# Kernel tuning notes

Hardware: AMD Instinct MI355X
Metric: run time of the kernel (lower is better)

Reference implementation:

```python
import jax, jax.numpy as jnp
import numpy as np

P = 2            # power (even positive int)
TEMPERATURE = 1.0
SCALE = 1.0 / np.sqrt(64.0)  # sqrt(head_dim) scaling
EPS = 1e-6


def setup_inputs() -> dict:
    key = jax.random.key(0)
    kq, kk, kv = jax.random.split(key, 3)
    shape = (4, 16, 2048, 64)  # (B, H, N, head_dim)
    return {
        "q": jax.random.normal(kq, shape, dtype=jnp.float32),
        "k": jax.random.normal(kk, shape, dtype=jnp.float32),
        "v": jax.random.normal(kv, shape, dtype=jnp.float32),
    }


def reference(q, k, v):
    # logits = q @ k^T * scale / temperature : (B, H, N, N)
    logits = jnp.einsum("bhnd,bhmd->bhnm", q, k) * (SCALE / TEMPERATURE)
    attn = logits ** P
    attn = attn / (attn.sum(axis=-1, keepdims=True) + EPS)
    return jnp.einsum("bhnm,bhmd->bhnd", attn, v)
```

## Files before the change

### kernel.cpp

```cpp
#include <hip/hip_runtime.h>

#define N_CTX 2048
#define DHEAD 64
#define SCALE_F 0.125f
#define EPS_F 1e-6f
#define KT 64
#define NITER (N_CTX / KT)
#define QBLK 256

typedef __attribute__((ext_vector_type(8))) short short8;
typedef __attribute__((ext_vector_type(4))) short short4v;
typedef __attribute__((ext_vector_type(4))) float float4v;
typedef __attribute__((ext_vector_type(2))) unsigned uint2v;
typedef __attribute__((ext_vector_type(4))) unsigned uint4v;

#if defined(__HIP_DEVICE_COMPILE__) && __has_builtin(__builtin_amdgcn_cvt_pk_bf16_f32)
typedef __attribute__((ext_vector_type(2))) __bf16 bf16x2;
__device__ __forceinline__ unsigned pack2(float a, float b) {
    union { bf16x2 v; unsigned u; } x;
    x.v = __builtin_amdgcn_cvt_pk_bf16_f32(a, b);
    return x.u;
}
#else
__device__ __forceinline__ unsigned bf1(float f) {
    union { float f; unsigned u; } x; x.f = f;
    return (x.u + 0x7FFFu + ((x.u >> 16) & 1u)) >> 16;
}
__device__ __forceinline__ unsigned pack2(float a, float b) {
    return bf1(a) | (bf1(b) << 16);
}
#endif

#if defined(__HIP_DEVICE_COMPILE__)
  #if __has_builtin(__builtin_amdgcn_mfma_f32_16x16x16bf16_1k)
    #define MFMA16(a, b, c) __builtin_amdgcn_mfma_f32_16x16x16bf16_1k(a, b, c, 0, 0, 0)
  #elif __has_builtin(__builtin_amdgcn_mfma_f32_16x16x16_bf16_1k)
    #define MFMA16(a, b, c) __builtin_amdgcn_mfma_f32_16x16x16_bf16_1k(a, b, c, 0, 0, 0)
  #else
    __device__ __forceinline__ float4v mfma16_asm(short4v a, short4v b, float4v c) {
        asm volatile("v_mfma_f32_16x16x16_bf16 %0, %1, %2, %0"
                     : "+v"(c) : "v"(a), "v"(b));
        return c;
    }
    #define MFMA16(a, b, c) mfma16_asm(a, b, c)
  #endif
#else
  #define MFMA16(a, b, c) (c)
#endif


__global__ __launch_bounds__(256, 2)
void powsm_attn(const float* __restrict__ qg, const float* __restrict__ kg,
                const float* __restrict__ vg, float* __restrict__ og)
{
    __shared__ short Ks[64][72];
    __shared__ short Vt[64][68];
    __shared__ float Dn[4][64];

    const int bh   = blockIdx.y;
    const int tid  = threadIdx.x;
    const int wave = tid >> 6;
    const int lane = tid & 63;
    const int qd   = lane >> 4;
    const int c    = lane & 15;

    const size_t base = (size_t)bh * N_CTX * DHEAD;
    const float* qp = qg + base;
    const float* kp = kg + base;
    const float* vp = vg + base;
    float*       op = og + base;

    const int qw0 = blockIdx.x * QBLK + wave * 64;

    short8 Qf[4][2];
    #pragma unroll
    for (int qt = 0; qt < 4; ++qt) {
        #pragma unroll
        for (int ks = 0; ks < 2; ++ks) {
            const float* src = qp + (size_t)(qw0 + qt*16 + c) * DHEAD + ks*32 + qd*8;
            float4v a = *(const float4v*)(src);
            float4v b = *(const float4v*)(src + 4);
            uint4v u;
            u[0] = pack2(a[0]*SCALE_F, a[1]*SCALE_F);
            u[1] = pack2(a[2]*SCALE_F, a[3]*SCALE_F);
            u[2] = pack2(b[0]*SCALE_F, b[1]*SCALE_F);
            u[3] = pack2(b[2]*SCALE_F, b[3]*SCALE_F);
            union { uint4v u; short8 s; } cv; cv.u = u;
            Qf[qt][ks] = cv.s;
        }
    }

    float4v Oacc[4][4];
    #pragma unroll
    for (int qt = 0; qt < 4; ++qt)
        #pragma unroll
        for (int nt = 0; nt < 4; ++nt)
            Oacc[qt][nt] = (float4v){0.f, 0.f, 0.f, 0.f};
    float4v dacc[4];
    #pragma unroll
    for (int qt = 0; qt < 4; ++qt) dacc[qt] = (float4v){0.f, 0.f, 0.f, 0.f};

    const int kr = tid >> 4;
    const int kc = tid & 15;

    float4v pK[4], pV[4];
    #pragma unroll
    for (int u = 0; u < 4; ++u)
        pK[u] = *(const float4v*)(kp + (size_t)(kr + u*16) * DHEAD + kc*4);
    #pragma unroll
    for (int j = 0; j < 4; ++j)
        pV[j] = *(const float4v*)(vp + (size_t)(4*kr + j) * DHEAD + kc*4);

    #pragma unroll 1
    for (int kvi = 0; kvi < NITER; ++kvi) {
        __syncthreads();

        #pragma unroll
        for (int u = 0; u < 4; ++u) {
            uint2v w; w[0] = pack2(pK[u][0], pK[u][1]); w[1] = pack2(pK[u][2], pK[u][3]);
            *(uint2v*)&Ks[kr + u*16][kc*4] = w;
        }
        #pragma unroll
        for (int kk = 0; kk < 4; ++kk) {
            uint2v w; w[0] = pack2(pV[0][kk], pV[1][kk]); w[1] = pack2(pV[2][kk], pV[3][kk]);
            *(uint2v*)&Vt[4*kc + kk][4*kr] = w;
        }
        __syncthreads();

        if (kvi + 1 < NITER) {
            const float* kn = kp + (size_t)(kvi + 1) * KT * DHEAD;
            const float* vn = vp + (size_t)(kvi + 1) * KT * DHEAD;
            #pragma unroll
            for (int u = 0; u < 4; ++u)
                pK[u] = *(const float4v*)(kn + (size_t)(kr + u*16) * DHEAD + kc*4);
            #pragma unroll
            for (int j = 0; j < 4; ++j)
                pV[j] = *(const float4v*)(vn + (size_t)(4*kr + j) * DHEAD + kc*4);
        }

        #pragma unroll
        for (int mt = 0; mt < 4; ++mt) {
            float4v s[4];
            #pragma unroll
            for (int qt = 0; qt < 4; ++qt) s[qt] = (float4v){0.f, 0.f, 0.f, 0.f};
            #pragma unroll
            for (int ks = 0; ks < 2; ++ks) {
                short8 af = *(const short8*)&Ks[mt*16 + c][ks*32 + qd*8];
                #pragma unroll
                for (int qt = 0; qt < 4; ++qt)
                    s[qt] = __builtin_amdgcn_mfma_f32_16x16x32_bf16(af, Qf[qt][ks], s[qt], 0, 0, 0);
            }
            short4v pa[4];
            #pragma unroll
            for (int qt = 0; qt < 4; ++qt) {
                float p0 = s[qt][0]*s[qt][0], p1 = s[qt][1]*s[qt][1];
                float p2 = s[qt][2]*s[qt][2], p3 = s[qt][3]*s[qt][3];
                dacc[qt][0] += p0; dacc[qt][1] += p1;
                dacc[qt][2] += p2; dacc[qt][3] += p3;
                union { uint2v u; short4v s; } cv;
                cv.u[0] = pack2(p0, p1); cv.u[1] = pack2(p2, p3);
                pa[qt] = cv.s;
            }
            #pragma unroll
            for (int nt = 0; nt < 4; ++nt) {
                short4v bf = *(const short4v*)&Vt[nt*16 + c][mt*16 + qd*4];
                #pragma unroll
                for (int qt = 0; qt < 4; ++qt)
                    Oacc[qt][nt] = MFMA16(pa[qt], bf, Oacc[qt][nt]);
            }
        }
    }

    #pragma unroll
    for (int qt = 0; qt < 4; ++qt) {
        float d = (dacc[qt][0] + dacc[qt][1]) + (dacc[qt][2] + dacc[qt][3]);
        d += __shfl_xor(d, 16);
        d += __shfl_xor(d, 32);
        if (qd == 0) Dn[wave][qt*16 + c] = d;
    }
    __syncthreads();

    #pragma unroll
    for (int qt = 0; qt < 4; ++qt) {
        #pragma unroll
        for (int r = 0; r < 4; ++r) {
            float inv = 1.0f / (Dn[wave][qt*16 + qd*4 + r] + EPS_F);
            float* dst = op + (size_t)(qw0 + qt*16 + qd*4 + r) * DHEAD + c;
            #pragma unroll
            for (int nt = 0; nt < 4; ++nt)
                dst[nt*16] = Oacc[qt][nt][r] * inv;
        }
    }
}

extern "C" void kernel_launch(void* const* d_in, const int* in_sizes, int n_in,
                              void* d_out, int out_size, void* d_ws, size_t ws_size,
                              hipStream_t stream) {
    const float* q = (const float*)d_in[0];
    const float* k = (const float*)d_in[1];
    const float* v = (const float*)d_in[2];
    float* out = (float*)d_out;
    dim3 grid(N_CTX / QBLK, 64, 1);
    powsm_attn<<<grid, dim3(256, 1, 1), 0, stream>>>(q, k, v, out);
}
```

Before: 209.4 us.

## Double-buffer K/V tiles and use 16x16x32 MFMA for PV via permlane swaps

Replaces the 16x16x16 bf16 MFMA in the P·V product with the wider 16x16x32 instruction. The P operand layout is rearranged with permlane32/permlane16 swaps so two 16-key score tiles form one 32-key A operand. It also double-buffers the K and V shared-memory tiles, so each iteration needs one barrier instead of two and the next tile's stores come after compute. This halves PV MFMA issue count and removes a sync, at the cost of extra LDS and permute instructions whose lane mapping must be exactly right.

```diff
diff --git a/kernel.cpp b/kernel.cpp
--- a/kernel.cpp
+++ b/kernel.cpp
@@ -9,7 +9,6 @@
 #define QBLK 256
 
 typedef __attribute__((ext_vector_type(8))) short short8;
-typedef __attribute__((ext_vector_type(4))) short short4v;
 typedef __attribute__((ext_vector_type(4))) float float4v;
 typedef __attribute__((ext_vector_type(2))) unsigned uint2v;
 typedef __attribute__((ext_vector_type(4))) unsigned uint4v;
@@ -31,21 +30,25 @@
 }
 #endif
 
-#if defined(__HIP_DEVICE_COMPILE__)
-  #if __has_builtin(__builtin_amdgcn_mfma_f32_16x16x16bf16_1k)
-    #define MFMA16(a, b, c) __builtin_amdgcn_mfma_f32_16x16x16bf16_1k(a, b, c, 0, 0, 0)
-  #elif __has_builtin(__builtin_amdgcn_mfma_f32_16x16x16_bf16_1k)
-    #define MFMA16(a, b, c) __builtin_amdgcn_mfma_f32_16x16x16_bf16_1k(a, b, c, 0, 0, 0)
-  #else
-    __device__ __forceinline__ float4v mfma16_asm(short4v a, short4v b, float4v c) {
-        asm volatile("v_mfma_f32_16x16x16_bf16 %0, %1, %2, %0"
-                     : "+v"(c) : "v"(a), "v"(b));
-        return c;
-    }
-    #define MFMA16(a, b, c) mfma16_asm(a, b, c)
-  #endif
+#if defined(__HIP_DEVICE_COMPILE__) && __has_builtin(__builtin_amdgcn_permlane32_swap)
+__device__ __forceinline__ void pl32(unsigned &x, unsigned &y) {
+    uint2v r = __builtin_amdgcn_permlane32_swap(x, y, false, false);
+    x = r[0]; y = r[1];
+}
 #else
-  #define MFMA16(a, b, c) (c)
+__device__ __forceinline__ void pl32(unsigned &x, unsigned &y) {
+    asm volatile("v_permlane32_swap_b32 %0, %1" : "+v"(x), "+v"(y));
+}
+#endif
+#if defined(__HIP_DEVICE_COMPILE__) && __has_builtin(__builtin_amdgcn_permlane16_swap)
+__device__ __forceinline__ void pl16(unsigned &x, unsigned &y) {
+    uint2v r = __builtin_amdgcn_permlane16_swap(x, y, false, false);
+    x = r[0]; y = r[1];
+}
+#else
+__device__ __forceinline__ void pl16(unsigned &x, unsigned &y) {
+    asm volatile("v_permlane16_swap_b32 %0, %1" : "+v"(x), "+v"(y));
+}
 #endif
 
 
@@ -53,8 +56,8 @@
 void powsm_attn(const float* __restrict__ qg, const float* __restrict__ kg,
                 const float* __restrict__ vg, float* __restrict__ og)
 {
-    __shared__ short Ks[64][72];
-    __shared__ short Vt[64][68];
+    __shared__ __align__(16) short KsB[2][64][72];
+    __shared__ __align__(16) short VtB[2][64][72];
     __shared__ float Dn[4][64];
 
     const int bh   = blockIdx.y;
@@ -111,10 +114,9 @@
     for (int j = 0; j < 4; ++j)
         pV[j] = *(const float4v*)(vp + (size_t)(4*kr + j) * DHEAD + kc*4);
 
-    #pragma unroll 1
-    for (int kvi = 0; kvi < NITER; ++kvi) {
-        __syncthreads();
-
+    {
+        short (*Ks)[72] = KsB[0];
+        short (*Vt)[72] = VtB[0];
         #pragma unroll
         for (int u = 0; u < 4; ++u) {
             uint2v w; w[0] = pack2(pK[u][0], pK[u][1]); w[1] = pack2(pK[u][2], pK[u][3]);
@@ -125,7 +127,14 @@
             uint2v w; w[0] = pack2(pV[0][kk], pV[1][kk]); w[1] = pack2(pV[2][kk], pV[3][kk]);
             *(uint2v*)&Vt[4*kc + kk][4*kr] = w;
         }
-        __syncthreads();
+    }
+    __syncthreads();
+
+    #pragma unroll 1
+    for (int kvi = 0; kvi < NITER; ++kvi) {
+        const int cur = kvi & 1;
+        short (*Ks)[72] = KsB[cur];
+        short (*Vt)[72] = VtB[cur];
 
         if (kvi + 1 < NITER) {
             const float* kn = kp + (size_t)(kvi + 1) * KT * DHEAD;
@@ -135,40 +144,76 @@
                 pK[u] = *(const float4v*)(kn + (size_t)(kr + u*16) * DHEAD + kc*4);
             #pragma unroll
             for (int j = 0; j < 4; ++j)
-                pV[j] = *(const float4v*)(vn + (size_t)(4*kr + j) * DHEAD + kc*4);
-        }
-
-        #pragma unroll
-        for (int mt = 0; mt < 4; ++mt) {
-            float4v s[4];
-            #pragma unroll
-            for (int qt = 0; qt < 4; ++qt) s[qt] = (float4v){0.f, 0.f, 0.f, 0.f};
+                pV[j] = *(const float4v*)(vn + (size_t)(2*kr*2 + j) * DHEAD + kc*4);
+        }
+
+        #pragma unroll
+        for (int blk = 0; blk < 2; ++blk) {
+            float4v slo[4], shi[4];
+            #pragma unroll
+            for (int qt = 0; qt < 4; ++qt) {
+                slo[qt] = (float4v){0.f, 0.f, 0.f, 0.f};
+                shi[qt] = (float4v){0.f, 0.f, 0.f, 0.f};
+            }
             #pragma unroll
             for (int ks = 0; ks < 2; ++ks) {
-                short8 af = *(const short8*)&Ks[mt*16 + c][ks*32 + qd*8];
+                short8 afl = *(const short8*)&Ks[blk*32 + c][ks*32 + qd*8];
                 #pragma unroll
                 for (int qt = 0; qt < 4; ++qt)
-                    s[qt] = __builtin_amdgcn_mfma_f32_16x16x32_bf16(af, Qf[qt][ks], s[qt], 0, 0, 0);
-            }
-            short4v pa[4];
-            #pragma unroll
-            for (int qt = 0; qt < 4; ++qt) {
-                float p0 = s[qt][0]*s[qt][0], p1 = s[qt][1]*s[qt][1];
-                float p2 = s[qt][2]*s[qt][2], p3 = s[qt][3]*s[qt][3];
-                dacc[qt][0] += p0; dacc[qt][1] += p1;
-                dacc[qt][2] += p2; dacc[qt][3] += p3;
-                union { uint2v u; short4v s; } cv;
-                cv.u[0] = pack2(p0, p1); cv.u[1] = pack2(p2, p3);
-                pa[qt] = cv.s;
-            }
-            #pragma unroll
-            for (int nt = 0; nt < 4; ++nt) {
-                short4v bf = *(const short4v*)&Vt[nt*16 + c][mt*16 + qd*4];
+                    slo[qt] = __builtin_amdgcn_mfma_f32_16x16x32_bf16(afl, Qf[qt][ks], slo[qt], 0, 0, 0);
+            }
+            #pragma unroll
+            for (int ks = 0; ks < 2; ++ks) {
+                short8 afh = *(const short8*)&Ks[blk*32 + 16 + c][ks*32 + qd*8];
                 #pragma unroll
                 for (int qt = 0; qt < 4; ++qt)
-                    Oacc[qt][nt] = MFMA16(pa[qt], bf, Oacc[qt][nt]);
-            }
-        }
+                    shi[qt] = __builtin_amdgcn_mfma_f32_16x16x32_bf16(afh, Qf[qt][ks], shi[qt], 0, 0, 0);
+            }
+            short8 pa[4];
+            #pragma unroll
+            for (int qt = 0; qt < 4; ++qt) {
+                float l0 = slo[qt][0]*slo[qt][0], l1 = slo[qt][1]*slo[qt][1];
+                float l2 = slo[qt][2]*slo[qt][2], l3 = slo[qt][3]*slo[qt][3];
+                float h0 = shi[qt][0]*shi[qt][0], h1 = shi[qt][1]*shi[qt][1];
+                float h2 = shi[qt][2]*shi[qt][2], h3 = shi[qt][3]*shi[qt][3];
+                dacc[qt][0] += l0 + h0; dacc[qt][1] += l1 + h1;
+                dacc[qt][2] += l2 + h2; dacc[qt][3] += l3 + h3;
+                unsigned w00 = pack2(l0, l1);
+                unsigned w01 = pack2(l2, l3);
+                unsigned w10 = pack2(h0, h1);
+                unsigned w11 = pack2(h2, h3);
+                pl32(w00, w10);
+                pl32(w01, w11);
+                pl16(w00, w10);
+                pl16(w01, w11);
+                union { uint4v u; short8 s; } cv;
+                cv.u[0] = w00; cv.u[1] = w01; cv.u[2] = w10; cv.u[3] = w11;
+                pa[qt] = cv.s;
+            }
+            #pragma unroll
+            for (int nt = 0; nt < 4; ++nt) {
+                short8 bf = *(const short8*)&Vt[nt*16 + c][blk*32 + qd*8];
+                #pragma unroll
+                for (int qt = 0; qt < 4; ++qt)
+                    Oacc[qt][nt] = __builtin_amdgcn_mfma_f32_16x16x32_bf16(pa[qt], bf, Oacc[qt][nt], 0, 0, 0);
+            }
+        }
+
+        if (kvi + 1 < NITER) {
+            short (*Kn)[72] = KsB[cur ^ 1];
+            short (*Vn)[72] = VtB[cur ^ 1];
+            #pragma unroll
+            for (int u = 0; u < 4; ++u) {
+                uint2v w; w[0] = pack2(pK[u][0], pK[u][1]); w[1] = pack2(pK[u][2], pK[u][3]);
+                *(uint2v*)&Kn[kr + u*16][kc*4] = w;
+            }
+            #pragma unroll
+            for (int kk = 0; kk < 4; ++kk) {
+                uint2v w; w[0] = pack2(pV[0][kk], pV[1][kk]); w[1] = pack2(pV[2][kk], pV[3][kk]);
+                *(uint2v*)&Vn[4*kc + kk][4*kr] = w;
+            }
+        }
+        __syncthreads();
     }
 
     #pragma unroll
```

After: 205.0 us. -2.1%, faster.
